# Performance work log

Hardware: AMD Instinct MI355X
Metric: run time of the kernel (lower is better)

The kernel has to match this reference:

```python
import jax, jax.numpy as jnp
import numpy as np

# E2M1 (FP4) value table: low 3 bits magnitude, bit 3 sign (indices 8..15 negative)
FP4_TABLE = jnp.array([0.0, 0.5, 1.0, 1.5, 2.0, 3.0, 4.0, 6.0,
                       0.0, -0.5, -1.0, -1.5, -2.0, -3.0, -4.0, -6.0], dtype=jnp.float32)
FP4_BLOCK = 32  # per-row 1x32 scale groups


def dequant_fp4(packed, scale):
    """packed: [E, O, I//2] uint8 (two e2m1 nibbles per byte, low nibble first),
    scale: [E, O, I//32] float32 (e8m0, i.e. powers of two). Returns [E, O, I] float32."""
    lo = (packed & 15).astype(jnp.int32)
    hi = ((packed >> 4) & 15).astype(jnp.int32)
    # interleave low, high nibbles along the input dim (matches torch stack(...,-1).flatten)
    vals = FP4_TABLE[jnp.stack([lo, hi], axis=-1)]  # [E, O, I//2, 2]
    w = vals.reshape(packed.shape[0], packed.shape[1], packed.shape[2] * 2)
    return w * jnp.repeat(scale, FP4_BLOCK, axis=-1)


def setup_inputs() -> dict:
    T, H, F, E, K = 2048, 2048, 1024, 16, 4
    key = jax.random.key(0)
    k = jax.random.split(key, 8)
    hidden_states = jax.random.normal(k[0], (T, H), dtype=jnp.float32)
    topk_weights = jax.nn.softmax(jax.random.normal(k[1], (T, K)), axis=-1)
    topk_ids = jax.random.randint(k[2], (T, K), 0, E, dtype=jnp.int32)
    # checkpoint-native packed FP4 expert weights + e8m0 (power-of-two) scales
    gate_up_weight = jax.random.randint(k[3], (E, 2 * F, H // 2), 0, 256, dtype=jnp.int32).astype(jnp.uint8)
    gate_up_scale = jnp.exp2(jax.random.randint(k[4], (E, 2 * F, H // 32), -8, -5).astype(jnp.float32))
    down_weight = jax.random.randint(k[5], (E, H, F // 2), 0, 256, dtype=jnp.int32).astype(jnp.uint8)
    down_scale = jnp.exp2(jax.random.randint(k[6], (E, H, F // 32), -8, -5).astype(jnp.float32))
    return {"hidden_states": hidden_states, "topk_weights": topk_weights, "topk_ids": topk_ids,
            "gate_up_weight": gate_up_weight, "gate_up_scale": gate_up_scale,
            "down_weight": down_weight, "down_scale": down_scale}


def reference(hidden_states, topk_weights, topk_ids, gate_up_weight, gate_up_scale, down_weight, down_scale):
    # 1. dequantize checkpoint-native FP4 experts to dense float weights
    w_gate_up = dequant_fp4(gate_up_weight, gate_up_scale)  # [E, 2F, H]
    w_down = dequant_fp4(down_weight, down_scale)           # [E, H, F]
    T = hidden_states.shape[0]
    E = w_gate_up.shape[0]
    # 2. scatter routing weights into a dense [T, E] combine matrix
    combine = jnp.zeros((T, E), dtype=hidden_states.dtype)
    combine = combine.at[jnp.arange(T)[:, None], topk_ids].add(topk_weights)
    # 3. grouped expert GEMM (exact dense dispatch over experts)
    gu = jnp.einsum('th,eoh->teo', hidden_states, w_gate_up)  # [T, E, 2F]
    gate, up = jnp.split(gu, 2, axis=-1)                       # gate = first ffn_dim rows
    act = jax.nn.silu(gate) * up                               # SwiGLU (swiglu_limit=0 -> no clamping)
    act = act * combine[:, :, None]                            # fold routing weights into activations
    return jnp.einsum('tef,ehf->th', act, w_down)              # [T, H]
```

## Files before the change

kernel.cpp:

```cpp
#include <hip/hip_runtime.h>
#include <stdint.h>

#define HD 2048
#define FD 1024
#define NE 16
#define NPAIR 8192
#define BM 256
#define MAXT 48

typedef short bf16x8 __attribute__((ext_vector_type(8)));
typedef float f32x4 __attribute__((ext_vector_type(4)));
typedef unsigned short u16;

static __device__ __forceinline__ u16 f2bf(float f) {
  uint32_t u = __float_as_uint(f);
  u += 0x7FFFu + ((u >> 16) & 1u);
  return (u16)(u >> 16);
}

struct DqTab { uint32_t hA, hB, lA, lB; };

static __device__ __forceinline__ DqTab make_tab(uint32_t sbits) {
  int n = (int)(sbits >> 23) - 127;
  int q = n >> 1;
  uint32_t r = (uint32_t)(n & 1);
  uint32_t mq = (uint32_t)(-q);
  uint32_t sub1 = mq * 0x01010100u;
  uint32_t subA = mq * 0x01010101u;
  DqTab t;
  t.hA = (r ? 0x40403F00u : 0x3F3F3F00u) - sub1;
  t.hB = (r ? 0x41414040u : 0x40404040u) - subA;
  t.lA = r ? 0x40008000u : 0xC0800000u;
  t.lB = r ? 0x4000C080u : 0xC0804000u;
  return t;
}

static __device__ __forceinline__ void dq8(uint32_t p, const DqTab& t, uint32_t* d) {
  uint32_t a = p & 0x0F0F0F0Fu;
  uint32_t b = (p >> 4) & 0x0F0F0F0Fu;
  uint32_t x0 = __builtin_amdgcn_perm(b, a, 0x05010400u);
  uint32_t x1 = __builtin_amdgcn_perm(b, a, 0x07030602u);
  uint32_t m0 = x0 & 0x07070707u;
  uint32_t m1 = x1 & 0x07070707u;
  uint32_t h0 = __builtin_amdgcn_perm(t.hB, t.hA, m0) | ((x0 & 0x08080808u) << 4);
  uint32_t h1 = __builtin_amdgcn_perm(t.hB, t.hA, m1) | ((x1 & 0x08080808u) << 4);
  uint32_t l0 = __builtin_amdgcn_perm(t.lB, t.lA, m0);
  uint32_t l1 = __builtin_amdgcn_perm(t.lB, t.lA, m1);
  d[0] = __builtin_amdgcn_perm(h0, l0, 0x05010400u);
  d[1] = __builtin_amdgcn_perm(h0, l0, 0x07030602u);
  d[2] = __builtin_amdgcn_perm(h1, l1, 0x05010400u);
  d[3] = __builtin_amdgcn_perm(h1, l1, 0x07030602u);
}

static __device__ __forceinline__ uint32_t pack4(int4 v) {
  return (uint32_t)(v.x & 0xFF) | ((uint32_t)(v.y & 0xFF) << 8) |
         ((uint32_t)(v.z & 0xFF) << 16) | ((uint32_t)v.w << 24);
}

static __device__ __forceinline__ bf16x8 dqfrag(const uint32_t* pB, const uint32_t* pS,
                                                int row, int j, int q) {
  uint32_t pb = pB[row * 9 + j * 4 + q];
  DqTab t = make_tab(pS[row * 2 + j]);
  uint32_t d[4];
  dq8(pb, t, d);
  union { uint32_t u[4]; bf16x8 v; } cv;
  cv.u[0] = d[0]; cv.u[1] = d[1]; cv.u[2] = d[2]; cv.u[3] = d[3];
  return cv.v;
}

static __device__ __forceinline__ void glds16(const void* g, void* l) {
  __builtin_amdgcn_global_load_lds(
      (const __attribute__((address_space(1))) uint32_t*)g,
      (__attribute__((address_space(3))) uint32_t*)l, 16, 0, 0);
}

__global__ void cast_kernel(const float* __restrict__ x, u16* __restrict__ xb) {
  int i = blockIdx.x * 256 + threadIdx.x;
  float4 v = ((const float4*)x)[i];
  ushort4 o;
  o.x = f2bf(v.x); o.y = f2bf(v.y); o.z = f2bf(v.z); o.w = f2bf(v.w);
  ((ushort4*)xb)[i] = o;
}

__global__ void zero_kernel(float4* __restrict__ out) {
  out[blockIdx.x * 256 + threadIdx.x] = float4{0.f, 0.f, 0.f, 0.f};
}

__global__ void route_kernel(const int* __restrict__ ids, const float* __restrict__ tw,
                             int* __restrict__ rows, float* __restrict__ rw,
                             int* __restrict__ te, int* __restrict__ pidx) {
  __shared__ int cnt[NE], base[NE], run[NE];
  int tid = threadIdx.x;
  if (tid < NE) { cnt[tid] = 0; run[tid] = 0; }
  __syncthreads();
  for (int i = tid; i < NPAIR; i += 256) atomicAdd(&cnt[ids[i]], 1);
  __syncthreads();
  if (tid == 0) {
    int cum = 0;
    for (int e = 0; e < NE; ++e) {
      base[e] = cum;
      int nt = (cnt[e] + BM - 1) >> 8;
      for (int j = 0; j < nt; ++j) te[(cum >> 8) + j] = e;
      cum += nt << 8;
    }
    for (int t = cum >> 8; t < MAXT; ++t) te[t] = -1;
  }
  __syncthreads();
  for (int i = tid; i < MAXT * BM; i += 256) {
    rows[i] = -1;
    rw[i] = 0.f;
    if (pidx) pidx[i] = -1;
  }
  __syncthreads();
  for (int i = tid; i < NPAIR; i += 256) {
    int e = ids[i];
    int p = base[e] + atomicAdd(&run[e], 1);
    rows[p] = i >> 2;
    rw[p] = tw[i];
    if (pidx) pidx[p] = i;
  }
}

__global__ __launch_bounds__(256, 2) void gemm1_kernel(
    const u16* __restrict__ xb, const int* __restrict__ gup32,
    const uint32_t* __restrict__ gus, const int* __restrict__ rows,
    const float* __restrict__ rw, const int* __restrict__ te,
    u16* __restrict__ act) {
  const int tile = blockIdx.y;
  const int e = te[tile];
  if (e < 0) return;
  const int f0 = blockIdx.x * 64;

  __shared__ u16 sA[2][BM * 64];
  __shared__ uint32_t sBp[2][128 * 9];
  __shared__ uint32_t sSc[2][256];
  __shared__ int rows_s[BM];
  __shared__ float rw_s[BM];

  const int tid = threadIdx.x;
  rows_s[tid] = rows[tile * BM + tid];
  rw_s[tid] = rw[tile * BM + tid];
  __syncthreads();

  const int lane = tid & 63;
  const int w = tid >> 6;
  const int q = lane >> 4, c = lane & 15;

  uint32_t aofs[8];
#pragma unroll
  for (int i = 0; i < 8; ++i) {
    const int lrow = w * 64 + i * 8 + (lane >> 3);
    int grow = rows_s[lrow];
    grow = grow < 0 ? 0 : grow;
    aofs[i] = (uint32_t)grow * HD + (uint32_t)(((lane & 7) ^ (lrow & 7)) << 3);
  }

  uint32_t obj[4];
#pragma unroll
  for (int j = 0; j < 4; ++j) {
    const int r_ = (tid >> 3) + j * 32;
    const int o_ = r_ < 64 ? f0 + r_ : 1024 + f0 + (r_ - 64);
    obj[j] = (uint32_t)(e * 2048 + o_) * 1024 + (uint32_t)((tid & 7) << 2);
  }
  const int r_sc = tid >> 1;
  const int o_sc = r_sc < 64 ? f0 + r_sc : 1024 + f0 + (r_sc - 64);
  const uint32_t scb = (uint32_t)(e * 2048 + o_sc) * 64 + (uint32_t)(tid & 1);

  const int x0 = ((q * 16) ^ ((c & 7) << 4)) >> 1;
  const int x1 = ((64 + q * 16) ^ ((c & 7) << 4)) >> 1;

  f32x4 Cg[4][4], Cu[4][4];
#pragma unroll
  for (int s = 0; s < 4; ++s)
#pragma unroll
    for (int t2 = 0; t2 < 4; ++t2) {
      Cg[s][t2] = f32x4{0.f, 0.f, 0.f, 0.f};
      Cu[s][t2] = f32x4{0.f, 0.f, 0.f, 0.f};
    }

  int4 breg[4];
  uint32_t sreg;

  {
#pragma unroll
    for (int i = 0; i < 8; ++i)
      glds16(xb + aofs[i], &sA[0][(w * 64 + i * 8) * 64]);
    int4 b0[4];
#pragma unroll
    for (int j = 0; j < 4; ++j) b0[j] = *(const int4*)(gup32 + obj[j]);
    uint32_t s0 = gus[scb];
#pragma unroll
    for (int j = 0; j < 4; ++j)
      sBp[0][((tid >> 3) + j * 32) * 9 + (tid & 7)] = pack4(b0[j]);
    sSc[0][tid] = s0;
#pragma unroll
    for (int j = 0; j < 4; ++j) breg[j] = *(const int4*)(gup32 + obj[j] + 32);
    sreg = gus[scb + 2];
    __syncthreads();
  }

  for (int s = 0; s < 32; ++s) {
    const int cur = s & 1;
    if (s < 31) {
#pragma unroll
      for (int i = 0; i < 8; ++i)
        glds16(xb + aofs[i] + (uint32_t)(s + 1) * 64, &sA[cur ^ 1][(w * 64 + i * 8) * 64]);
#pragma unroll
      for (int j = 0; j < 4; ++j)
        sBp[cur ^ 1][((tid >> 3) + j * 32) * 9 + (tid & 7)] = pack4(breg[j]);
      sSc[cur ^ 1][tid] = sreg;
    }
    if (s < 30) {
#pragma unroll
      for (int j = 0; j < 4; ++j)
        breg[j] = *(const int4*)(gup32 + obj[j] + (uint32_t)(s + 2) * 32);
      sreg = gus[scb + (uint32_t)(s + 2) * 2];
    }
#pragma unroll
    for (int j = 0; j < 2; ++j) {
      const int xo = j ? x1 : x0;
      bf16x8 af[4];
#pragma unroll
      for (int s4 = 0; s4 < 4; ++s4)
        af[s4] = *(const bf16x8*)&sA[cur][(w * 64 + s4 * 16 + c) * 64 + xo];
#pragma unroll
      for (int t2 = 0; t2 < 4; ++t2) {
        bf16x8 bg = dqfrag(sBp[cur], sSc[cur], t2 * 16 + c, j, q);
        bf16x8 bu = dqfrag(sBp[cur], sSc[cur], 64 + t2 * 16 + c, j, q);
#pragma unroll
        for (int s4 = 0; s4 < 4; ++s4) {
          Cg[s4][t2] = __builtin_amdgcn_mfma_f32_16x16x32_bf16(af[s4], bg, Cg[s4][t2], 0, 0, 0);
          Cu[s4][t2] = __builtin_amdgcn_mfma_f32_16x16x32_bf16(af[s4], bu, Cu[s4][t2], 0, 0, 0);
        }
      }
    }
    __syncthreads();
  }

#pragma unroll
  for (int s = 0; s < 4; ++s) {
    const int mlb = w * 64 + s * 16 + q * 4;
#pragma unroll
    for (int t2 = 0; t2 < 4; ++t2) {
      const int fg = f0 + t2 * 16 + c;
#pragma unroll
      for (int r = 0; r < 4; ++r) {
        const int ml = mlb + r;
        float g = Cg[s][t2][r];
        float u = Cu[s][t2][r];
        float aval = g / (1.f + __expf(-g)) * u * rw_s[ml];
        act[(size_t)(tile * BM + ml) * FD + fg] = f2bf(aval);
      }
    }
  }
}

__global__ __launch_bounds__(256, 2) void gemm2_kernel(
    const u16* __restrict__ act, const int* __restrict__ dwn32,
    const uint32_t* __restrict__ dsc, const int* __restrict__ rows,
    const int* __restrict__ pidx, const int* __restrict__ te,
    float* __restrict__ out, float* __restrict__ pout) {
  const int tile = blockIdx.y;
  const int e = te[tile];
  if (e < 0) return;
  const int h0 = blockIdx.x * 128;

  __shared__ u16 sA[2][BM * 64];
  __shared__ uint32_t sBp[2][128 * 9];
  __shared__ uint32_t sSc[2][256];
  __shared__ int rows_s[BM];
  __shared__ int pidx_s[BM];

  const int tid = threadIdx.x;
  rows_s[tid] = rows[tile * BM + tid];
  pidx_s[tid] = pout ? pidx[tile * BM + tid] : -1;
  __syncthreads();

  const int lane = tid & 63;
  const int w = tid >> 6;
  const int q = lane >> 4, c = lane & 15;

  uint32_t aofs[8];
#pragma unroll
  for (int i = 0; i < 8; ++i) {
    const int lrow = w * 64 + i * 8 + (lane >> 3);
    aofs[i] = (uint32_t)(tile * BM + lrow) * FD + (uint32_t)(((lane & 7) ^ (lrow & 7)) << 3);
  }

  uint32_t obj[4];
#pragma unroll
  for (int j = 0; j < 4; ++j) {
    const int r_ = (tid >> 3) + j * 32;
    obj[j] = (uint32_t)(e * 2048 + h0 + r_) * 512 + (uint32_t)((tid & 7) << 2);
  }
  const uint32_t scb = (uint32_t)(e * 2048 + h0 + (tid >> 1)) * 32 + (uint32_t)(tid & 1);

  const int x0 = ((q * 16) ^ ((c & 7) << 4)) >> 1;
  const int x1 = ((64 + q * 16) ^ ((c & 7) << 4)) >> 1;

  f32x4 Cd[4][8];
#pragma unroll
  for (int s = 0; s < 4; ++s)
#pragma unroll
    for (int t2 = 0; t2 < 8; ++t2) Cd[s][t2] = f32x4{0.f, 0.f, 0.f, 0.f};

  int4 breg[4];
  uint32_t sreg;

  {
#pragma unroll
    for (int i = 0; i < 8; ++i)
      glds16(act + aofs[i], &sA[0][(w * 64 + i * 8) * 64]);
    int4 b0[4];
#pragma unroll
    for (int j = 0; j < 4; ++j) b0[j] = *(const int4*)(dwn32 + obj[j]);
    uint32_t s0 = dsc[scb];
#pragma unroll
    for (int j = 0; j < 4; ++j)
      sBp[0][((tid >> 3) + j * 32) * 9 + (tid & 7)] = pack4(b0[j]);
    sSc[0][tid] = s0;
#pragma unroll
    for (int j = 0; j < 4; ++j) breg[j] = *(const int4*)(dwn32 + obj[j] + 32);
    sreg = dsc[scb + 2];
    __syncthreads();
  }

  for (int s = 0; s < 16; ++s) {
    const int cur = s & 1;
    if (s < 15) {
#pragma unroll
      for (int i = 0; i < 8; ++i)
        glds16(act + aofs[i] + (uint32_t)(s + 1) * 64, &sA[cur ^ 1][(w * 64 + i * 8) * 64]);
#pragma unroll
      for (int j = 0; j < 4; ++j)
        sBp[cur ^ 1][((tid >> 3) + j * 32) * 9 + (tid & 7)] = pack4(breg[j]);
      sSc[cur ^ 1][tid] = sreg;
    }
    if (s < 14) {
#pragma unroll
      for (int j = 0; j < 4; ++j)
        breg[j] = *(const int4*)(dwn32 + obj[j] + (uint32_t)(s + 2) * 32);
      sreg = dsc[scb + (uint32_t)(s + 2) * 2];
    }
#pragma unroll
    for (int j = 0; j < 2; ++j) {
      const int xo = j ? x1 : x0;
      bf16x8 af[4];
#pragma unroll
      for (int s4 = 0; s4 < 4; ++s4)
        af[s4] = *(const bf16x8*)&sA[cur][(w * 64 + s4 * 16 + c) * 64 + xo];
#pragma unroll
      for (int t2 = 0; t2 < 8; ++t2) {
        bf16x8 bf_ = dqfrag(sBp[cur], sSc[cur], t2 * 16 + c, j, q);
#pragma unroll
        for (int s4 = 0; s4 < 4; ++s4)
          Cd[s4][t2] = __builtin_amdgcn_mfma_f32_16x16x32_bf16(af[s4], bf_, Cd[s4][t2], 0, 0, 0);
      }
    }
    __syncthreads();
  }

  if (pout) {
#pragma unroll
    for (int s = 0; s < 4; ++s) {
      const int mlb = w * 64 + s * 16 + q * 4;
#pragma unroll
      for (int t2 = 0; t2 < 8; ++t2) {
        const int hg = h0 + t2 * 16 + c;
#pragma unroll
        for (int r = 0; r < 4; ++r) {
          int prow = pidx_s[mlb + r];
          if (prow >= 0) pout[(size_t)prow * HD + hg] = Cd[s][t2][r];
        }
      }
    }
  } else {
#pragma unroll
    for (int s = 0; s < 4; ++s) {
      const int mlb = w * 64 + s * 16 + q * 4;
#pragma unroll
      for (int t2 = 0; t2 < 8; ++t2) {
        const int hg = h0 + t2 * 16 + c;
#pragma unroll
        for (int r = 0; r < 4; ++r) {
          int token = rows_s[mlb + r];
          if (token >= 0) atomicAdd(&out[(size_t)token * HD + hg], Cd[s][t2][r]);
        }
      }
    }
  }
}

__global__ void finalize_kernel(const float4* __restrict__ pout, float4* __restrict__ out) {
  int j = blockIdx.x * 256 + threadIdx.x;
  int token = j >> 9;
  int col = j & 511;
  const float4* p = pout + ((size_t)token * 4) * 512 + col;
  float4 a = p[0], b = p[512], c = p[1024], d = p[1536];
  out[j] = float4{a.x + b.x + c.x + d.x, a.y + b.y + c.y + d.y,
                  a.z + b.z + c.z + d.z, a.w + b.w + c.w + d.w};
}

extern "C" void kernel_launch(void* const* d_in, const int* in_sizes, int n_in,
                              void* d_out, int out_size, void* d_ws, size_t ws_size,
                              hipStream_t stream) {
  const float* hidden = (const float*)d_in[0];
  const float* tw = (const float*)d_in[1];
  const int* ids = (const int*)d_in[2];
  const int* gup32 = (const int*)d_in[3];
  const uint32_t* gus = (const uint32_t*)d_in[4];
  const int* dwn32 = (const int*)d_in[5];
  const uint32_t* dsc = (const uint32_t*)d_in[6];
  float* out = (float*)d_out;

  char* ws = (char*)d_ws;
  int* rows = (int*)(ws);
  float* rw = (float*)(ws + 49152);
  int* te = (int*)(ws + 98304);
  u16* xb = (u16*)(ws + 131072);
  u16* act = (u16*)(ws + 8519680);

  const size_t POUT_OFF = 33685504ULL;
  const size_t PIDX_OFF = POUT_OFF + (size_t)NPAIR * HD * 4;
  const size_t WS_NEED = PIDX_OFF + (size_t)MAXT * BM * 4;
  const bool big = ws_size >= WS_NEED;
  float* pout = big ? (float*)(ws + POUT_OFF) : nullptr;
  int* pidx = big ? (int*)(ws + PIDX_OFF) : nullptr;

  cast_kernel<<<dim3(4096), dim3(256), 0, stream>>>(hidden, xb);
  if (!big) zero_kernel<<<dim3(4096), dim3(256), 0, stream>>>((float4*)out);
  route_kernel<<<dim3(1), dim3(256), 0, stream>>>(ids, tw, rows, rw, te, pidx);
  gemm1_kernel<<<dim3(16, MAXT), dim3(256), 0, stream>>>(xb, gup32, gus, rows, rw, te, act);
  gemm2_kernel<<<dim3(16, MAXT), dim3(256), 0, stream>>>(act, dwn32, dsc, rows, pidx, te, out, pout);
  if (big) finalize_kernel<<<dim3(1024 * 1024 / 256), dim3(256), 0, stream>>>((const float4*)pout, (float4*)out);
}
```

Before: 539.2 us.

## Split warp tiles 2x2 so each warp dequantizes fewer B fragments

Both GEMM kernels change warp layout from 4 row-strips (64 rows x full N each) to a 2x2 grid (128 rows x half N). Each warp now dequantizes half as many FP4 B fragments per k-step and reads twice as many A fragments from LDS, cutting the ALU dequant work that was duplicated across all four warps. The cost is more LDS A reads per warp and a different accumulator shape, which may change register pressure.

```diff
diff --git a/kernel.cpp b/kernel.cpp
--- a/kernel.cpp
+++ b/kernel.cpp
@@ -144,6 +144,8 @@
 
   const int lane = tid & 63;
   const int w = tid >> 6;
+  const int wr = w >> 1;
+  const int wc = w & 1;
   const int q = lane >> 4, c = lane & 15;
 
   uint32_t aofs[8];
@@ -169,11 +171,11 @@
   const int x0 = ((q * 16) ^ ((c & 7) << 4)) >> 1;
   const int x1 = ((64 + q * 16) ^ ((c & 7) << 4)) >> 1;
 
-  f32x4 Cg[4][4], Cu[4][4];
-#pragma unroll
-  for (int s = 0; s < 4; ++s)
-#pragma unroll
-    for (int t2 = 0; t2 < 4; ++t2) {
+  f32x4 Cg[8][2], Cu[8][2];
+#pragma unroll
+  for (int s = 0; s < 8; ++s)
+#pragma unroll
+    for (int t2 = 0; t2 < 2; ++t2) {
       Cg[s][t2] = f32x4{0.f, 0.f, 0.f, 0.f};
       Cu[s][t2] = f32x4{0.f, 0.f, 0.f, 0.f};
     }
@@ -219,18 +221,19 @@
 #pragma unroll
     for (int j = 0; j < 2; ++j) {
       const int xo = j ? x1 : x0;
-      bf16x8 af[4];
-#pragma unroll
-      for (int s4 = 0; s4 < 4; ++s4)
-        af[s4] = *(const bf16x8*)&sA[cur][(w * 64 + s4 * 16 + c) * 64 + xo];
-#pragma unroll
-      for (int t2 = 0; t2 < 4; ++t2) {
-        bf16x8 bg = dqfrag(sBp[cur], sSc[cur], t2 * 16 + c, j, q);
-        bf16x8 bu = dqfrag(sBp[cur], sSc[cur], 64 + t2 * 16 + c, j, q);
-#pragma unroll
-        for (int s4 = 0; s4 < 4; ++s4) {
-          Cg[s4][t2] = __builtin_amdgcn_mfma_f32_16x16x32_bf16(af[s4], bg, Cg[s4][t2], 0, 0, 0);
-          Cu[s4][t2] = __builtin_amdgcn_mfma_f32_16x16x32_bf16(af[s4], bu, Cu[s4][t2], 0, 0, 0);
+      bf16x8 bg[2], bu[2];
+#pragma unroll
+      for (int t2 = 0; t2 < 2; ++t2) {
+        bg[t2] = dqfrag(sBp[cur], sSc[cur], wc * 32 + t2 * 16 + c, j, q);
+        bu[t2] = dqfrag(sBp[cur], sSc[cur], 64 + wc * 32 + t2 * 16 + c, j, q);
+      }
+#pragma unroll
+      for (int s4 = 0; s4 < 8; ++s4) {
+        bf16x8 af = *(const bf16x8*)&sA[cur][(wr * 128 + s4 * 16 + c) * 64 + xo];
+#pragma unroll
+        for (int t2 = 0; t2 < 2; ++t2) {
+          Cg[s4][t2] = __builtin_amdgcn_mfma_f32_16x16x32_bf16(af, bg[t2], Cg[s4][t2], 0, 0, 0);
+          Cu[s4][t2] = __builtin_amdgcn_mfma_f32_16x16x32_bf16(af, bu[t2], Cu[s4][t2], 0, 0, 0);
         }
       }
     }
@@ -238,16 +241,16 @@
   }
 
 #pragma unroll
-  for (int s = 0; s < 4; ++s) {
-    const int mlb = w * 64 + s * 16 + q * 4;
-#pragma unroll
-    for (int t2 = 0; t2 < 4; ++t2) {
-      const int fg = f0 + t2 * 16 + c;
+  for (int s4 = 0; s4 < 8; ++s4) {
+    const int mlb = wr * 128 + s4 * 16 + q * 4;
+#pragma unroll
+    for (int t2 = 0; t2 < 2; ++t2) {
+      const int fg = f0 + wc * 32 + t2 * 16 + c;
 #pragma unroll
       for (int r = 0; r < 4; ++r) {
         const int ml = mlb + r;
-        float g = Cg[s][t2][r];
-        float u = Cu[s][t2][r];
+        float g = Cg[s4][t2][r];
+        float u = Cu[s4][t2][r];
         float aval = g / (1.f + __expf(-g)) * u * rw_s[ml];
         act[(size_t)(tile * BM + ml) * FD + fg] = f2bf(aval);
       }
@@ -278,6 +281,8 @@
 
   const int lane = tid & 63;
   const int w = tid >> 6;
+  const int wr = w >> 1;
+  const int wc = w & 1;
   const int q = lane >> 4, c = lane & 15;
 
   uint32_t aofs[8];
@@ -298,11 +303,11 @@
   const int x0 = ((q * 16) ^ ((c & 7) << 4)) >> 1;
   const int x1 = ((64 + q * 16) ^ ((c & 7) << 4)) >> 1;
 
-  f32x4 Cd[4][8];
-#pragma unroll
-  for (int s = 0; s < 4; ++s)
-#pragma unroll
-    for (int t2 = 0; t2 < 8; ++t2) Cd[s][t2] = f32x4{0.f, 0.f, 0.f, 0.f};
+  f32x4 Cd[8][4];
+#pragma unroll
+  for (int s = 0; s < 8; ++s)
+#pragma unroll
+    for (int t2 = 0; t2 < 4; ++t2) Cd[s][t2] = f32x4{0.f, 0.f, 0.f, 0.f};
 
   int4 breg[4];
   uint32_t sreg;
@@ -345,16 +350,16 @@
 #pragma unroll
     for (int j = 0; j < 2; ++j) {
       const int xo = j ? x1 : x0;
-      bf16x8 af[4];
-#pragma unroll
-      for (int s4 = 0; s4 < 4; ++s4)
-        af[s4] = *(const bf16x8*)&sA[cur][(w * 64 + s4 * 16 + c) * 64 + xo];
-#pragma unroll
-      for (int t2 = 0; t2 < 8; ++t2) {
-        bf16x8 bf_ = dqfrag(sBp[cur], sSc[cur], t2 * 16 + c, j, q);
-#pragma unroll
-        for (int s4 = 0; s4 < 4; ++s4)
-          Cd[s4][t2] = __builtin_amdgcn_mfma_f32_16x16x32_bf16(af[s4], bf_, Cd[s4][t2], 0, 0, 0);
+      bf16x8 bf_[4];
+#pragma unroll
+      for (int t2 = 0; t2 < 4; ++t2)
+        bf_[t2] = dqfrag(sBp[cur], sSc[cur], wc * 64 + t2 * 16 + c, j, q);
+#pragma unroll
+      for (int s4 = 0; s4 < 8; ++s4) {
+        bf16x8 af = *(const bf16x8*)&sA[cur][(wr * 128 + s4 * 16 + c) * 64 + xo];
+#pragma unroll
+        for (int t2 = 0; t2 < 4; ++t2)
+          Cd[s4][t2] = __builtin_amdgcn_mfma_f32_16x16x32_bf16(af, bf_[t2], Cd[s4][t2], 0, 0, 0);
       }
     }
     __syncthreads();
@@ -362,29 +367,29 @@
 
   if (pout) {
 #pragma unroll
-    for (int s = 0; s < 4; ++s) {
-      const int mlb = w * 64 + s * 16 + q * 4;
-#pragma unroll
-      for (int t2 = 0; t2 < 8; ++t2) {
-        const int hg = h0 + t2 * 16 + c;
+    for (int s4 = 0; s4 < 8; ++s4) {
+      const int mlb = wr * 128 + s4 * 16 + q * 4;
+#pragma unroll
+      for (int t2 = 0; t2 < 4; ++t2) {
+        const int hg = h0 + wc * 64 + t2 * 16 + c;
 #pragma unroll
         for (int r = 0; r < 4; ++r) {
           int prow = pidx_s[mlb + r];
-          if (prow >= 0) pout[(size_t)prow * HD + hg] = Cd[s][t2][r];
+          if (prow >= 0) pout[(size_t)prow * HD + hg] = Cd[s4][t2][r];
         }
       }
     }
   } else {
 #pragma unroll
-    for (int s = 0; s < 4; ++s) {
-      const int mlb = w * 64 + s * 16 + q * 4;
-#pragma unroll
-      for (int t2 = 0; t2 < 8; ++t2) {
-        const int hg = h0 + t2 * 16 + c;
+    for (int s4 = 0; s4 < 8; ++s4) {
+      const int mlb = wr * 128 + s4 * 16 + q * 4;
+#pragma unroll
+      for (int t2 = 0; t2 < 4; ++t2) {
+        const int hg = h0 + wc * 64 + t2 * 16 + c;
 #pragma unroll
         for (int r = 0; r < 4; ++r) {
           int token = rows_s[mlb + r];
-          if (token >= 0) atomicAdd(&out[(size_t)token * HD + hg], Cd[s][t2][r]);
+          if (token >= 0) atomicAdd(&out[(size_t)token * HD + hg], Cd[s4][t2][r]);
         }
       }
     }
```

Result: faster. 495.0 us (-8.2%).
